# Kernel optimization log

Hardware: AMD Instinct MI355X
Metric: run time of the kernel (lower is better)

The kernel has to match this reference:

```python
import jax, jax.numpy as jnp
import numpy as np

WS, SHIFT, HEADS, FEAT = 7, 3, 3, 56
N = WS * WS

def _rel_pos_index(ws):
    coords = np.stack(np.meshgrid(np.arange(ws), np.arange(ws), indexing='ij'))  # 2,ws,ws
    coords = coords.reshape(2, -1)
    rel = coords[:, :, None] - coords[:, None, :]            # 2,N,N
    rel = rel.transpose(1, 2, 0).astype(np.int64)            # N,N,2
    rel[:, :, 0] += ws - 1
    rel[:, :, 1] += ws - 1
    rel[:, :, 0] *= 2 * ws - 1
    return rel.sum(-1)                                       # N,N in [0,(2ws-1)^2)

def _shift_mask(H, ws, shift):
    img = np.zeros((H, H), dtype=np.float32)
    cnt = 0
    for hs in (slice(0, -ws), slice(-ws, -shift), slice(-shift, None)):
        for wl in (slice(0, -ws), slice(-ws, -shift), slice(-shift, None)):
            img[hs, wl] = cnt
            cnt += 1
    win = img.reshape(H // ws, ws, H // ws, ws).transpose(0, 2, 1, 3).reshape(-1, ws * ws)
    diff = win[:, None, :] - win[:, :, None]                 # nW,N,N (unsqueeze(1)-unsqueeze(2))
    return np.where(diff != 0, -100.0, 0.0).astype(np.float32)

_REL_IDX = jnp.asarray(_rel_pos_index(WS))
_MASK = jnp.asarray(_shift_mask(FEAT, WS, SHIFT))            # (nW_per_img, N, N)

def setup_inputs() -> dict:
    key = jax.random.key(0)
    ks = jax.random.split(key, 4)
    C = 96
    return {
        'x': jax.random.normal(ks[0], (128, C, FEAT, FEAT), jnp.float32),
        'ln_g': jnp.ones((C,), jnp.float32),
        'ln_b': jnp.zeros((C,), jnp.float32),
        'qkv_w': jax.random.normal(ks[1], (3 * C, C), jnp.float32) * 0.02,
        'qkv_b': jnp.zeros((3 * C,), jnp.float32),
        'proj_w': jax.random.normal(ks[2], (C, C), jnp.float32) * 0.02,
        'proj_b': jnp.zeros((C,), jnp.float32),
        'rel_table': jax.random.normal(ks[3], ((2 * WS - 1) ** 2, HEADS), jnp.float32) * 0.02,
    }

def reference(x, ln_g, ln_b, qkv_w, qkv_b, proj_w, proj_b, rel_table):
    B, C, H, W = x.shape
    hd = C // HEADS
    nwh = H // WS
    # BCHW -> BHWC, LayerNorm over C
    xt = x.transpose(0, 2, 3, 1)
    mu = xt.mean(-1, keepdims=True)
    var = ((xt - mu) ** 2).mean(-1, keepdims=True)
    xn = (xt - mu) * jax.lax.rsqrt(var + 1e-5) * ln_g + ln_b
    # cyclic shift
    xn = jnp.roll(xn, (-SHIFT, -SHIFT), axis=(1, 2))
    # window partition -> (B*nW, N, C)
    win = xn.reshape(B, nwh, WS, nwh, WS, C).transpose(0, 1, 3, 2, 4, 5).reshape(-1, N, C)
    # qkv
    qkv = (win @ qkv_w.T + qkv_b).reshape(-1, N, 3, HEADS, hd).transpose(2, 0, 3, 1, 4)
    q, k, v = qkv[0], qkv[1], qkv[2]                         # (B*nW, heads, N, hd)
    attn = jnp.einsum('whid,whjd->whij', q * (hd ** -0.5), k)
    bias = rel_table[_REL_IDX].transpose(2, 0, 1)            # heads,N,N
    attn = attn + bias[None]
    nWp = nwh * nwh
    attn = attn.reshape(B, nWp, HEADS, N, N) + _MASK[None, :, None]
    attn = jax.nn.softmax(attn, axis=-1).reshape(-1, HEADS, N, N)
    out = jnp.einsum('whij,whjd->whid', attn, v).transpose(0, 2, 1, 3).reshape(-1, N, C)
    out = out @ proj_w.T + proj_b
    # window reverse + unshift
    out = out.reshape(B, nwh, nwh, WS, WS, C).transpose(0, 1, 3, 2, 4, 5).reshape(B, H, W, C)
    out = jnp.roll(out, (SHIFT, SHIFT), axis=(1, 2))
    return out.transpose(0, 3, 1, 2)
```

## Files before the change

kernel.cpp:

```cpp
#include <hip/hip_runtime.h>

typedef unsigned short u16;
typedef __bf16 bf8v __attribute__((ext_vector_type(8)));
typedef float f4v __attribute__((ext_vector_type(4)));
typedef f4v __attribute__((may_alias)) f4va;

#define NTOK   49
#define NPAD   64
#define CDIM   96
#define FEAT_  56
#define HWIM   3136
#define SHIFT_ 3

#define WIN_ELEMS (128 * 64 * 49 * 96)
#define QW_ELEMS  (288 * 96)
#define PW_ELEMS  (96 * 96)
#define WS_NEEDED ((size_t)(WIN_ELEMS + QW_ELEMS + PW_ELEMS) * 2)

__device__ __forceinline__ float b2f(u16 u) {
  unsigned v = ((unsigned)u) << 16;
  return __builtin_bit_cast(float, v);
}
__device__ __forceinline__ u16 f2b(float f) {
  return __builtin_bit_cast(u16, (__bf16)f);
}
__device__ __forceinline__ bf8v fragld(const u16* p) {
  return __builtin_bit_cast(bf8v, *(const f4va*)p);
}
__device__ __forceinline__ bf8v cvt8(const float* p) {
  f4v a = *(const f4va*)p;
  f4v b = *(const f4va*)(p + 4);
  union { u16 u[8]; bf8v v; } r;
#pragma unroll
  for (int j = 0; j < 4; ++j) { r.u[j] = f2b(a[j]); r.u[4 + j] = f2b(b[j]); }
  return r.v;
}
__device__ __forceinline__ f4v mfma16(bf8v a, bf8v b, f4v c) {
  return __builtin_amdgcn_mfma_f32_16x16x32_bf16(a, b, c, 0, 0, 0);
}
__device__ __forceinline__ int reg3(int g) { return g < 49 ? 0 : (g < 53 ? 1 : 2); }

__global__ __launch_bounds__(256)
void swin_wcvt(const float* __restrict__ qw, const float* __restrict__ pw,
               u16* __restrict__ qwb, u16* __restrict__ pwb) {
  int i = blockIdx.x * 256 + threadIdx.x;
  if (i < QW_ELEMS) qwb[i] = f2b(qw[i]);
  else              pwb[i - QW_ELEMS] = f2b(pw[i - QW_ELEMS]);
}

__global__ __launch_bounds__(256, 4)
void swin_ln_pack(const float* __restrict__ x,
                  const float* __restrict__ lng, const float* __restrict__ lnb,
                  u16* __restrict__ winbuf) {
  __shared__ __align__(16) float xf[CDIM][60];
  __shared__ __align__(16) u16 wtile[FEAT_][104];
  __shared__ float ps[4][64], pq[4][64];
  __shared__ float gw[CDIM], bw[CDIM];

  const int bid = blockIdx.x;
  const int b = bid / FEAT_, hs = bid - b * FEAT_;
  int h = hs + SHIFT_; if (h >= FEAT_) h -= FEAT_;
  const int tid = threadIdx.x, wv = tid >> 6, lane = tid & 63;

  for (int i = tid; i < CDIM; i += 256) { gw[i] = lng[i]; bw[i] = lnb[i]; }

  const float* base = x + (size_t)b * CDIM * HWIM + h * FEAT_;
  if (lane < 56) {
    const int g = lane / 14, p4 = lane - g * 14;
    for (int i = 0; i < 6; ++i) {
      int c = wv * 24 + i * 4 + g;
      *(f4va*)&xf[c][p4 * 4] = *(const f4va*)(base + (size_t)c * HWIM + p4 * 4);
    }
  }
  __syncthreads();

  const int ws = lane;
  int wsrc = ws + SHIFT_; if (wsrc >= FEAT_) wsrc -= FEAT_;
  float s = 0.f, q = 0.f;
  if (ws < FEAT_)
    for (int i = 0; i < 24; ++i) {
      float v = xf[wv * 24 + i][wsrc];
      s += v; q += v * v;
    }
  ps[wv][lane] = s; pq[wv][lane] = q;
  __syncthreads();

  if (ws < FEAT_) {
    float ts = ps[0][ws] + ps[1][ws] + ps[2][ws] + ps[3][ws];
    float tq = pq[0][ws] + pq[1][ws] + pq[2][ws] + pq[3][ws];
    float m = ts * (1.f / 96.f);
    float r = rsqrtf(tq * (1.f / 96.f) - m * m + 1e-5f);
    for (int i = 0; i < 24; ++i) {
      int c = wv * 24 + i;
      wtile[ws][c] = f2b((xf[c][wsrc] - m) * r * gw[c] + bw[c]);
    }
  }
  __syncthreads();

  const int wrow = hs / 7, tr = hs - wrow * 7;
  for (int idx = tid; idx < 672; idx += 256) {
    int ww = idx / 84, r = idx - ww * 84;
    int wl = r / 12, cc = r - wl * 12;
    u16* dst = winbuf + ((size_t)((b * 64 + wrow * 8 + ww) * 49 + tr * 7)) * CDIM + r * 8;
    *(f4va*)dst = *(const f4va*)&wtile[ww * 7 + wl][cc * 8];
  }
}

__global__ __launch_bounds__(256, 3)
void swin_attn(u16* __restrict__ winbuf,
               const u16* __restrict__ qwb, const u16* __restrict__ pwb,
               const float* __restrict__ qbv, const float* __restrict__ pbv,
               const float* __restrict__ rel) {
  __shared__ __align__(16) u16 qk[NPAD][200];
  __shared__ __align__(16) u16 vt[3][32][72];
  __shared__ __align__(16) u16 Pl[NPAD][72];
  __shared__ float rel_f[507];
  __shared__ float pb_f[CDIM];
  __shared__ float qb_f[3 * CDIM];

  const int blk = blockIdx.x;
  const int wi = blk & 63;
  const int whb = wi >> 3, wwb = wi & 7;
  const int tid = threadIdx.x;
  const int wv = tid >> 6, lane = tid & 63;
  const int quad = lane >> 4, l15 = lane & 15;

  u16* wbase = winbuf + (size_t)blk * (NTOK * CDIM);

  for (int idx = tid; idx < 588; idx += 256) {
    int row = idx / 12, cc = idx - row * 12;
    *(f4va*)&qk[row][cc * 8] = *(const f4va*)(wbase + idx * 8);
  }
  {
    f4v z = {0.f, 0.f, 0.f, 0.f};
    for (int idx = tid; idx < 180; idx += 256) {
      int row = 49 + idx / 12, cc = idx - (idx / 12) * 12;
      *(f4va*)&qk[row][cc * 8] = z;
    }
  }
  for (int i = tid; i < 507; i += 256) rel_f[i] = rel[i];
  for (int i = tid; i < 3 * CDIM; i += 256) qb_f[i] = qbv[i];
  for (int i = tid; i < CDIM; i += 256) pb_f[i] = pbv[i];
  __syncthreads();

  {
    bf8v a[4][3];
    for (int mt = 0; mt < 4; ++mt)
      for (int kt = 0; kt < 3; ++kt)
        a[mt][kt] = fragld(&qk[mt * 16 + l15][kt * 32 + quad * 8]);
    __syncthreads();
    const float qscale = 0.17677669529663687f;
    for (int nt = wv; nt < 18; nt += 4) {
      int n = nt * 16 + l15;
      bf8v bf[3];
      for (int kt = 0; kt < 3; ++kt)
        bf[kt] = fragld(qwb + n * CDIM + kt * 32 + quad * 8);
      float bias = qb_f[n];
      for (int mt = 0; mt < 4; ++mt) {
        f4v c = {0.f, 0.f, 0.f, 0.f};
        c = mfma16(a[mt][0], bf[0], c);
        c = mfma16(a[mt][1], bf[1], c);
        c = mfma16(a[mt][2], bf[2], c);
        for (int rg = 0; rg < 4; ++rg) {
          int m = mt * 16 + quad * 4 + rg;
          float v = c[rg] + bias;
          if (n < 96)        qk[m][n] = f2b(v * qscale);
          else if (n < 192)  qk[m][n] = f2b(v);
          else               vt[(n - 192) >> 5][(n - 192) & 31][m] = f2b(v);
        }
      }
    }
  }
  __syncthreads();

  {
    const int rbase = wv * 16 + quad * 4;
    int rcnt[4], ri_[4], ci_[4];
    for (int rg = 0; rg < 4; ++rg) {
      int r = rbase + rg; if (r > 48) r = 48;
      int ri = r / 7, ci = r - ri * 7;
      ri_[rg] = ri; ci_[rg] = ci;
      rcnt[rg] = reg3(whb * 7 + ri) * 3 + reg3(wwb * 7 + ci);
    }
    int ib_[4][4]; float ms_[4][4]; bool jv_[4];
    for (int nt = 0; nt < 4; ++nt) {
      int j = nt * 16 + l15;
      jv_[nt] = (j < NTOK);
      int rj = j / 7, cj = j - rj * 7;
      int jcnt = reg3(whb * 7 + rj) * 3 + reg3(wwb * 7 + cj);
      for (int rg = 0; rg < 4; ++rg) {
        ib_[nt][rg] = ((ri_[rg] - rj + 6) * 13 + (ci_[rg] - cj + 6)) * 3;
        ms_[nt][rg] = (jcnt != rcnt[rg]) ? -100.f : 0.f;
      }
    }
    for (int h = 0; h < 3; ++h) {
      bf8v aq = fragld(&qk[wv * 16 + l15][h * 32 + quad * 8]);
      f4v S[4];
      for (int nt = 0; nt < 4; ++nt) {
        bf8v bk = fragld(&qk[nt * 16 + l15][96 + h * 32 + quad * 8]);
        f4v z = {0.f, 0.f, 0.f, 0.f};
        S[nt] = mfma16(aq, bk, z);
      }
      for (int nt = 0; nt < 4; ++nt) {
        if (jv_[nt]) {
          for (int rg = 0; rg < 4; ++rg)
            S[nt][rg] += rel_f[ib_[nt][rg] + h] + ms_[nt][rg];
        } else {
          for (int rg = 0; rg < 4; ++rg) S[nt][rg] = -1e30f;
        }
      }
      float inv[4];
      for (int rg = 0; rg < 4; ++rg) {
        float m = fmaxf(fmaxf(S[0][rg], S[1][rg]), fmaxf(S[2][rg], S[3][rg]));
        for (int off = 1; off < 16; off <<= 1) m = fmaxf(m, __shfl_xor(m, off, 64));
        float s = 0.f;
        for (int nt = 0; nt < 4; ++nt) {
          float e = __expf(S[nt][rg] - m); S[nt][rg] = e; s += e;
        }
        for (int off = 1; off < 16; off <<= 1) s += __shfl_xor(s, off, 64);
        inv[rg] = 1.f / s;
      }
      for (int nt = 0; nt < 4; ++nt) {
        int j = nt * 16 + l15;
        for (int rg = 0; rg < 4; ++rg)
          Pl[rbase + rg][j] = f2b(S[nt][rg] * inv[rg]);
      }
      bf8v ap0 = fragld(&Pl[wv * 16 + l15][quad * 8]);
      bf8v ap1 = fragld(&Pl[wv * 16 + l15][32 + quad * 8]);
      for (int nt = 0; nt < 2; ++nt) {
        bf8v bv0 = fragld(&vt[h][nt * 16 + l15][quad * 8]);
        bf8v bv1 = fragld(&vt[h][nt * 16 + l15][32 + quad * 8]);
        f4v c = {0.f, 0.f, 0.f, 0.f};
        c = mfma16(ap0, bv0, c);
        c = mfma16(ap1, bv1, c);
        for (int rg = 0; rg < 4; ++rg)
          qk[rbase + rg][h * 32 + nt * 16 + l15] = f2b(c[rg]);
      }
    }
  }
  __syncthreads();

  {
    bf8v a[4][3];
    for (int mt = 0; mt < 4; ++mt)
      for (int kt = 0; kt < 3; ++kt)
        a[mt][kt] = fragld(&qk[mt * 16 + l15][kt * 32 + quad * 8]);
    __syncthreads();
    for (int nt = wv; nt < 6; nt += 4) {
      int n = nt * 16 + l15;
      bf8v bf[3];
      for (int kt = 0; kt < 3; ++kt)
        bf[kt] = fragld(pwb + n * CDIM + kt * 32 + quad * 8);
      float bias = pb_f[n];
      for (int mt = 0; mt < 4; ++mt) {
        f4v c = {0.f, 0.f, 0.f, 0.f};
        c = mfma16(a[mt][0], bf[0], c);
        c = mfma16(a[mt][1], bf[1], c);
        c = mfma16(a[mt][2], bf[2], c);
        for (int rg = 0; rg < 4; ++rg)
          qk[mt * 16 + quad * 4 + rg][n] = f2b(c[rg] + bias);
      }
    }
  }
  __syncthreads();

  for (int idx = tid; idx < 588; idx += 256) {
    int row = idx / 12, cc = idx - row * 12;
    *(f4va*)(wbase + idx * 8) = *(const f4va*)&qk[row][cc * 8];
  }
}

__global__ __launch_bounds__(256, 4)
void swin_unpack(const u16* __restrict__ winbuf, float* __restrict__ out) {
  __shared__ __align__(16) u16 wtile[FEAT_][104];
  const int bid = blockIdx.x;
  const int b = bid / FEAT_, h = bid - b * FEAT_;
  int hs = h - SHIFT_; if (hs < 0) hs += FEAT_;
  const int wrow = hs / 7, tr = hs - wrow * 7;
  const int tid = threadIdx.x, wv = tid >> 6, lane = tid & 63;

  for (int idx = tid; idx < 672; idx += 256) {
    int ww = idx / 84, r = idx - ww * 84;
    const u16* src = winbuf + ((size_t)((b * 64 + wrow * 8 + ww) * 49 + tr * 7)) * CDIM + r * 8;
    int wl = r / 12, cc = r - wl * 12;
    int ws = ww * 7 + wl;
    int w = ws + SHIFT_; if (w >= FEAT_) w -= FEAT_;
    *(f4va*)&wtile[w][cc * 8] = *(const f4va*)src;
  }
  __syncthreads();
  if (lane < 56) {
    const int g = lane / 14, p4 = lane - g * 14;
    float* obase = out + (size_t)b * CDIM * HWIM + h * FEAT_ + p4 * 4;
    for (int i = 0; i < 6; ++i) {
      int c = wv * 24 + i * 4 + g;
      f4v v;
#pragma unroll
      for (int j = 0; j < 4; ++j) v[j] = b2f(wtile[p4 * 4 + j][c]);
      *(f4va*)(obase + (size_t)c * HWIM) = v;
    }
  }
}

__global__ __launch_bounds__(256, 2)
void swin_fused_fb(const float* __restrict__ x,
                   const float* __restrict__ lng, const float* __restrict__ lnb,
                   const float* __restrict__ qw,  const float* __restrict__ qbv,
                   const float* __restrict__ pw,  const float* __restrict__ pbv,
                   const float* __restrict__ rel,
                   float* __restrict__ out) {
  __shared__ union { float xf[NTOK][97]; u16 qk[NPAD][200]; } A;
  __shared__ union { u16 win16[NPAD][104]; u16 outb[NPAD][98]; } Bu;
  __shared__ u16 vt[3][32][72];
  __shared__ u16 Pl[NPAD][72];
  __shared__ u16 att[NPAD][104];
  __shared__ float gw[CDIM], bwt[CDIM];
  __shared__ float rel_f[507];
  __shared__ float pb_f[CDIM];
  __shared__ float qb_f[3 * CDIM];

  const int blk = blockIdx.x;
  const int b = blk >> 6, wi = blk & 63;
  const int whb = wi >> 3, wwb = wi & 7;
  const int tid = threadIdx.x, wv = tid >> 6, lane = tid & 63;
  const int quad = lane >> 4, l15 = lane & 15;
  {
    int p = lane;
    if (p < NTOK) {
      int r = p / 7, cw = p - r * 7;
      int h = whb * 7 + r + SHIFT_;  if (h >= FEAT_) h -= FEAT_;
      int w = wwb * 7 + cw + SHIFT_; if (w >= FEAT_) w -= FEAT_;
      const float* xp = x + b * CDIM * HWIM + h * FEAT_ + w;
      for (int c = wv; c < CDIM; c += 4) A.xf[p][c] = xp[c * HWIM];
    }
    for (int i = tid; i < CDIM; i += 256) { gw[i] = lng[i]; bwt[i] = lnb[i]; pb_f[i] = pbv[i]; }
    for (int i = tid; i < 507; i += 256) rel_f[i] = rel[i];
    for (int i = tid; i < 3 * CDIM; i += 256) qb_f[i] = qbv[i];
  }
  __syncthreads();
  {
    int p = wv * 16 + (lane >> 2), cg = lane & 3;
    float s = 0.f, q = 0.f;
    if (p < NTOK)
      for (int i = 0; i < 24; ++i) { float v = A.xf[p][cg * 24 + i]; s += v; q += v * v; }
    s += __shfl_xor(s, 1, 64); s += __shfl_xor(s, 2, 64);
    q += __shfl_xor(q, 1, 64); q += __shfl_xor(q, 2, 64);
    float m = s * (1.f / 96.f);
    float r = rsqrtf(q * (1.f / 96.f) - m * m + 1e-5f);
    for (int i = 0; i < 24; ++i) {
      int c = cg * 24 + i;
      float v = (p < NTOK) ? (A.xf[p][c] - m) * r * gw[c] + bwt[c] : 0.f;
      Bu.win16[p][c] = f2b(v);
    }
  }
  __syncthreads();
  {
    bf8v a[4][3];
    for (int mt = 0; mt < 4; ++mt)
      for (int kt = 0; kt < 3; ++kt)
        a[mt][kt] = fragld(&Bu.win16[mt * 16 + l15][kt * 32 + quad * 8]);
    const float qscale = 0.17677669529663687f;
    for (int nt = wv; nt < 18; nt += 4) {
      int n = nt * 16 + l15;
      const float* wr = qw + n * CDIM;
      bf8v bf[3];
      for (int kt = 0; kt < 3; ++kt) bf[kt] = cvt8(wr + kt * 32 + quad * 8);
      float bias = qb_f[n];
      for (int mt = 0; mt < 4; ++mt) {
        f4v c = {0.f, 0.f, 0.f, 0.f};
        c = mfma16(a[mt][0], bf[0], c);
        c = mfma16(a[mt][1], bf[1], c);
        c = mfma16(a[mt][2], bf[2], c);
        for (int rg = 0; rg < 4; ++rg) {
          int m = mt * 16 + quad * 4 + rg;
          float v = c[rg] + bias;
          if (n < 96)        A.qk[m][n] = f2b(v * qscale);
          else if (n < 192)  A.qk[m][n] = f2b(v);
          else               vt[(n - 192) >> 5][(n - 192) & 31][m] = f2b(v);
        }
      }
    }
  }
  __syncthreads();
  {
    const int rbase = wv * 16 + quad * 4;
    int rcnt[4], ri_[4], ci_[4];
    for (int rg = 0; rg < 4; ++rg) {
      int r = rbase + rg; if (r > 48) r = 48;
      int ri = r / 7, ci = r - ri * 7;
      ri_[rg] = ri; ci_[rg] = ci;
      rcnt[rg] = reg3(whb * 7 + ri) * 3 + reg3(wwb * 7 + ci);
    }
    for (int h = 0; h < 3; ++h) {
      bf8v aq = fragld(&A.qk[wv * 16 + l15][h * 32 + quad * 8]);
      f4v S[4];
      for (int nt = 0; nt < 4; ++nt) {
        bf8v bk = fragld(&A.qk[nt * 16 + l15][96 + h * 32 + quad * 8]);
        f4v z = {0.f, 0.f, 0.f, 0.f};
        S[nt] = mfma16(aq, bk, z);
      }
      for (int nt = 0; nt < 4; ++nt) {
        int j = nt * 16 + l15;
        if (j < NTOK) {
          int rj = j / 7, cj = j - rj * 7;
          int jcnt = reg3(whb * 7 + rj) * 3 + reg3(wwb * 7 + cj);
          for (int rg = 0; rg < 4; ++rg) {
            float add = rel_f[((ri_[rg] - rj + 6) * 13 + (ci_[rg] - cj + 6)) * 3 + h];
            if (jcnt != rcnt[rg]) add -= 100.f;
            S[nt][rg] += add;
          }
        } else {
          for (int rg = 0; rg < 4; ++rg) S[nt][rg] = -1e30f;
        }
      }
      float inv[4];
      for (int rg = 0; rg < 4; ++rg) {
        float m = fmaxf(fmaxf(S[0][rg], S[1][rg]), fmaxf(S[2][rg], S[3][rg]));
        for (int off = 1; off < 16; off <<= 1) m = fmaxf(m, __shfl_xor(m, off, 64));
        float s = 0.f;
        for (int nt = 0; nt < 4; ++nt) { float e = __expf(S[nt][rg] - m); S[nt][rg] = e; s += e; }
        for (int off = 1; off < 16; off <<= 1) s += __shfl_xor(s, off, 64);
        inv[rg] = 1.f / s;
      }
      for (int nt = 0; nt < 4; ++nt) {
        int j = nt * 16 + l15;
        for (int rg = 0; rg < 4; ++rg) Pl[rbase + rg][j] = f2b(S[nt][rg] * inv[rg]);
      }
      bf8v ap0 = fragld(&Pl[wv * 16 + l15][quad * 8]);
      bf8v ap1 = fragld(&Pl[wv * 16 + l15][32 + quad * 8]);
      for (int nt = 0; nt < 2; ++nt) {
        bf8v bv0 = fragld(&vt[h][nt * 16 + l15][quad * 8]);
        bf8v bv1 = fragld(&vt[h][nt * 16 + l15][32 + quad * 8]);
        f4v c = {0.f, 0.f, 0.f, 0.f};
        c = mfma16(ap0, bv0, c);
        c = mfma16(ap1, bv1, c);
        for (int rg = 0; rg < 4; ++rg)
          att[rbase + rg][h * 32 + nt * 16 + l15] = f2b(c[rg]);
      }
    }
  }
  __syncthreads();
  {
    bf8v a[4][3];
    for (int mt = 0; mt < 4; ++mt)
      for (int kt = 0; kt < 3; ++kt)
        a[mt][kt] = fragld(&att[mt * 16 + l15][kt * 32 + quad * 8]);
    for (int nt = wv; nt < 6; nt += 4) {
      int n = nt * 16 + l15;
      const float* wr = pw + n * CDIM;
      bf8v bf[3];
      for (int kt = 0; kt < 3; ++kt) bf[kt] = cvt8(wr + kt * 32 + quad * 8);
      float bias = pb_f[n];
      for (int mt = 0; mt < 4; ++mt) {
        f4v c = {0.f, 0.f, 0.f, 0.f};
        c = mfma16(a[mt][0], bf[0], c);
        c = mfma16(a[mt][1], bf[1], c);
        c = mfma16(a[mt][2], bf[2], c);
        for (int rg = 0; rg < 4; ++rg)
          Bu.outb[mt * 16 + quad * 4 + rg][n] = f2b(c[rg] + bias);
      }
    }
  }
  __syncthreads();
  {
    int p = lane;
    if (p < NTOK) {
      int r = p / 7, cw = p - r * 7;
      int h = whb * 7 + r + SHIFT_;  if (h >= FEAT_) h -= FEAT_;
      int w = wwb * 7 + cw + SHIFT_; if (w >= FEAT_) w -= FEAT_;
      float* op = out + b * CDIM * HWIM + h * FEAT_ + w;
      for (int c = wv; c < CDIM; c += 4) op[c * HWIM] = b2f(Bu.outb[p][c]);
    }
  }
}

extern "C" void kernel_launch(void* const* d_in, const int* in_sizes, int n_in,
                              void* d_out, int out_size, void* d_ws, size_t ws_size,
                              hipStream_t stream) {
  (void)in_sizes; (void)n_in; (void)out_size;
  const float* x   = (const float*)d_in[0];
  const float* lng = (const float*)d_in[1];
  const float* lnb = (const float*)d_in[2];
  const float* qw  = (const float*)d_in[3];
  const float* qbv = (const float*)d_in[4];
  const float* pw  = (const float*)d_in[5];
  const float* pbv = (const float*)d_in[6];
  const float* rel = (const float*)d_in[7];
  float* out = (float*)d_out;

  if (ws_size >= WS_NEEDED) {
    u16* winbuf = (u16*)d_ws;
    u16* qwb = winbuf + WIN_ELEMS;
    u16* pwb = qwb + QW_ELEMS;
    swin_wcvt<<<dim3(144), dim3(256), 0, stream>>>(qw, pw, qwb, pwb);
    swin_ln_pack<<<dim3(128 * FEAT_), dim3(256), 0, stream>>>(x, lng, lnb, winbuf);
    swin_attn<<<dim3(8192), dim3(256), 0, stream>>>(winbuf, qwb, pwb, qbv, pbv, rel);
    swin_unpack<<<dim3(128 * FEAT_), dim3(256), 0, stream>>>(winbuf, out);
  } else {
    swin_fused_fb<<<dim3(8192), dim3(256), 0, stream>>>(x, lng, lnb, qw, qbv, pw, pbv, rel, out);
  }
}
```

Baseline: 495.4 us.

## Vectorize LDS stores via swapped MFMA operands, direct LN writes, permuted unpack tile

The LayerNorm pack kernel now writes normalized bf16 rows straight to global memory in 16-byte chunks, dropping the shared staging tile and one barrier, and spreads its input load over all threads. The attention kernel swaps MFMA operand order so each lane holds four consecutive columns, which allows packed 8-byte shared-memory stores for Q/K, P, attention output and projection output. The same change lets the softmax reduction use two cross-lane shuffles instead of four per row. The projection work is split evenly across the four waves, and the unpack kernel permutes its tile rows to cut LDS bank conflicts; occupancy hints are raised on the pack and unpack kernels.

```diff
diff --git a/kernel.cpp b/kernel.cpp
--- a/kernel.cpp
+++ b/kernel.cpp
@@ -4,6 +4,8 @@
 typedef __bf16 bf8v __attribute__((ext_vector_type(8)));
 typedef float f4v __attribute__((ext_vector_type(4)));
 typedef f4v __attribute__((may_alias)) f4va;
+typedef unsigned int u2v __attribute__((ext_vector_type(2)));
+typedef u2v __attribute__((may_alias)) u2va;
 
 #define NTOK   49
 #define NPAD   64
@@ -48,12 +50,11 @@
   else              pwb[i - QW_ELEMS] = f2b(pw[i - QW_ELEMS]);
 }
 
-__global__ __launch_bounds__(256, 4)
+__global__ __launch_bounds__(256, 6)
 void swin_ln_pack(const float* __restrict__ x,
                   const float* __restrict__ lng, const float* __restrict__ lnb,
                   u16* __restrict__ winbuf) {
   __shared__ __align__(16) float xf[CDIM][60];
-  __shared__ __align__(16) u16 wtile[FEAT_][104];
   __shared__ float ps[4][64], pq[4][64];
   __shared__ float gw[CDIM], bw[CDIM];
 
@@ -65,12 +66,9 @@
   for (int i = tid; i < CDIM; i += 256) { gw[i] = lng[i]; bw[i] = lnb[i]; }
 
   const float* base = x + (size_t)b * CDIM * HWIM + h * FEAT_;
-  if (lane < 56) {
-    const int g = lane / 14, p4 = lane - g * 14;
-    for (int i = 0; i < 6; ++i) {
-      int c = wv * 24 + i * 4 + g;
-      *(f4va*)&xf[c][p4 * 4] = *(const f4va*)(base + (size_t)c * HWIM + p4 * 4);
-    }
+  for (int idx = tid; idx < 1344; idx += 256) {
+    int c = idx / 14, p4 = idx - c * 14;
+    *(f4va*)&xf[c][p4 * 4] = *(const f4va*)(base + (size_t)c * HWIM + p4 * 4);
   }
   __syncthreads();
 
@@ -90,19 +88,17 @@
     float tq = pq[0][ws] + pq[1][ws] + pq[2][ws] + pq[3][ws];
     float m = ts * (1.f / 96.f);
     float r = rsqrtf(tq * (1.f / 96.f) - m * m + 1e-5f);
+    const int ww = ws / 7, wl = ws - ww * 7;
+    const int wrow = hs / 7, tr = hs - wrow * 7;
+    u16* dst = winbuf + ((size_t)((b * 64 + wrow * 8 + ww) * 49 + tr * 7 + wl)) * CDIM + wv * 24;
+    union { u16 u[24]; f4v d[3]; } pk;
+#pragma unroll
     for (int i = 0; i < 24; ++i) {
       int c = wv * 24 + i;
-      wtile[ws][c] = f2b((xf[c][wsrc] - m) * r * gw[c] + bw[c]);
-    }
-  }
-  __syncthreads();
-
-  const int wrow = hs / 7, tr = hs - wrow * 7;
-  for (int idx = tid; idx < 672; idx += 256) {
-    int ww = idx / 84, r = idx - ww * 84;
-    int wl = r / 12, cc = r - wl * 12;
-    u16* dst = winbuf + ((size_t)((b * 64 + wrow * 8 + ww) * 49 + tr * 7)) * CDIM + r * 8;
-    *(f4va*)dst = *(const f4va*)&wtile[ww * 7 + wl][cc * 8];
+      pk.u[i] = f2b((xf[c][wsrc] - m) * r * gw[c] + bw[c]);
+    }
+#pragma unroll
+    for (int j = 0; j < 3; ++j) *(f4va*)(dst + j * 8) = pk.d[j];
   }
 }
 
@@ -115,8 +111,8 @@
   __shared__ __align__(16) u16 vt[3][32][72];
   __shared__ __align__(16) u16 Pl[NPAD][72];
   __shared__ float rel_f[507];
-  __shared__ float pb_f[CDIM];
-  __shared__ float qb_f[3 * CDIM];
+  __shared__ __align__(16) float pb_f[CDIM];
+  __shared__ __align__(16) float qb_f[3 * CDIM];
 
   const int blk = blockIdx.x;
   const int wi = blk & 63;
@@ -155,86 +151,107 @@
       bf8v bf[3];
       for (int kt = 0; kt < 3; ++kt)
         bf[kt] = fragld(qwb + n * CDIM + kt * 32 + quad * 8);
-      float bias = qb_f[n];
-      for (int mt = 0; mt < 4; ++mt) {
-        f4v c = {0.f, 0.f, 0.f, 0.f};
-        c = mfma16(a[mt][0], bf[0], c);
-        c = mfma16(a[mt][1], bf[1], c);
-        c = mfma16(a[mt][2], bf[2], c);
-        for (int rg = 0; rg < 4; ++rg) {
-          int m = mt * 16 + quad * 4 + rg;
-          float v = c[rg] + bias;
-          if (n < 96)        qk[m][n] = f2b(v * qscale);
-          else if (n < 192)  qk[m][n] = f2b(v);
-          else               vt[(n - 192) >> 5][(n - 192) & 31][m] = f2b(v);
+      if (nt < 12) {
+        const int n0 = nt * 16 + quad * 4;
+        f4v bias = *(const f4va*)&qb_f[n0];
+        const bool isq = (nt < 6);
+        for (int mt = 0; mt < 4; ++mt) {
+          f4v c = {0.f, 0.f, 0.f, 0.f};
+          c = mfma16(bf[0], a[mt][0], c);
+          c = mfma16(bf[1], a[mt][1], c);
+          c = mfma16(bf[2], a[mt][2], c);
+          union { u16 u[4]; u2v d; } pk;
+#pragma unroll
+          for (int rg = 0; rg < 4; ++rg) {
+            float v = c[rg] + bias[rg];
+            if (isq) v *= qscale;
+            pk.u[rg] = f2b(v);
+          }
+          *(u2va*)&qk[mt * 16 + l15][n0] = pk.d;
         }
-      }
-    }
-  }
-  __syncthreads();
-
-  {
-    const int rbase = wv * 16 + quad * 4;
-    int rcnt[4], ri_[4], ci_[4];
-    for (int rg = 0; rg < 4; ++rg) {
-      int r = rbase + rg; if (r > 48) r = 48;
-      int ri = r / 7, ci = r - ri * 7;
-      ri_[rg] = ri; ci_[rg] = ci;
-      rcnt[rg] = reg3(whb * 7 + ri) * 3 + reg3(wwb * 7 + ci);
-    }
-    int ib_[4][4]; float ms_[4][4]; bool jv_[4];
-    for (int nt = 0; nt < 4; ++nt) {
-      int j = nt * 16 + l15;
-      jv_[nt] = (j < NTOK);
-      int rj = j / 7, cj = j - rj * 7;
-      int jcnt = reg3(whb * 7 + rj) * 3 + reg3(wwb * 7 + cj);
+      } else {
+        float bias = qb_f[n];
+        const int hd = (n - 192) >> 5, dc = (n - 192) & 31;
+        for (int mt = 0; mt < 4; ++mt) {
+          f4v c = {0.f, 0.f, 0.f, 0.f};
+          c = mfma16(a[mt][0], bf[0], c);
+          c = mfma16(a[mt][1], bf[1], c);
+          c = mfma16(a[mt][2], bf[2], c);
+          union { u16 u[4]; u2v d; } pk;
+#pragma unroll
+          for (int rg = 0; rg < 4; ++rg) pk.u[rg] = f2b(c[rg] + bias);
+          *(u2va*)&vt[hd][dc][mt * 16 + quad * 4] = pk.d;
+        }
+      }
+    }
+  }
+  __syncthreads();
+
+  {
+    const int mrow = wv * 16 + l15;
+    int mc = mrow > 48 ? 48 : mrow;
+    const int ri = mc / 7, ci = mc - ri * 7;
+    const int rcnt = reg3(whb * 7 + ri) * 3 + reg3(wwb * 7 + ci);
+    int ib_[4][4]; float ms_[4][4]; bool jv_[4][4];
+    for (int jt = 0; jt < 4; ++jt)
       for (int rg = 0; rg < 4; ++rg) {
-        ib_[nt][rg] = ((ri_[rg] - rj + 6) * 13 + (ci_[rg] - cj + 6)) * 3;
-        ms_[nt][rg] = (jcnt != rcnt[rg]) ? -100.f : 0.f;
-      }
-    }
+        int j = jt * 16 + quad * 4 + rg;
+        jv_[jt][rg] = (j < NTOK);
+        int jj = j > 48 ? 48 : j;
+        int rj = jj / 7, cj = jj - rj * 7;
+        int jcnt = reg3(whb * 7 + rj) * 3 + reg3(wwb * 7 + cj);
+        ib_[jt][rg] = ((ri - rj + 6) * 13 + (ci - cj + 6)) * 3;
+        ms_[jt][rg] = (jcnt != rcnt) ? -100.f : 0.f;
+      }
     for (int h = 0; h < 3; ++h) {
       bf8v aq = fragld(&qk[wv * 16 + l15][h * 32 + quad * 8]);
       f4v S[4];
-      for (int nt = 0; nt < 4; ++nt) {
-        bf8v bk = fragld(&qk[nt * 16 + l15][96 + h * 32 + quad * 8]);
+      for (int jt = 0; jt < 4; ++jt) {
+        bf8v bk = fragld(&qk[jt * 16 + l15][96 + h * 32 + quad * 8]);
         f4v z = {0.f, 0.f, 0.f, 0.f};
-        S[nt] = mfma16(aq, bk, z);
-      }
-      for (int nt = 0; nt < 4; ++nt) {
-        if (jv_[nt]) {
-          for (int rg = 0; rg < 4; ++rg)
-            S[nt][rg] += rel_f[ib_[nt][rg] + h] + ms_[nt][rg];
-        } else {
-          for (int rg = 0; rg < 4; ++rg) S[nt][rg] = -1e30f;
+        S[jt] = mfma16(bk, aq, z);
+      }
+      for (int jt = 0; jt < 4; ++jt)
+#pragma unroll
+        for (int rg = 0; rg < 4; ++rg) {
+          if (jv_[jt][rg]) S[jt][rg] += rel_f[ib_[jt][rg] + h] + ms_[jt][rg];
+          else             S[jt][rg] = -1e30f;
         }
-      }
-      float inv[4];
-      for (int rg = 0; rg < 4; ++rg) {
-        float m = fmaxf(fmaxf(S[0][rg], S[1][rg]), fmaxf(S[2][rg], S[3][rg]));
-        for (int off = 1; off < 16; off <<= 1) m = fmaxf(m, __shfl_xor(m, off, 64));
-        float s = 0.f;
-        for (int nt = 0; nt < 4; ++nt) {
-          float e = __expf(S[nt][rg] - m); S[nt][rg] = e; s += e;
-        }
-        for (int off = 1; off < 16; off <<= 1) s += __shfl_xor(s, off, 64);
-        inv[rg] = 1.f / s;
-      }
-      for (int nt = 0; nt < 4; ++nt) {
-        int j = nt * 16 + l15;
-        for (int rg = 0; rg < 4; ++rg)
-          Pl[rbase + rg][j] = f2b(S[nt][rg] * inv[rg]);
+      float mx0 = fmaxf(fmaxf(S[0][0], S[0][1]), fmaxf(S[0][2], S[0][3]));
+      float mx1 = fmaxf(fmaxf(S[1][0], S[1][1]), fmaxf(S[1][2], S[1][3]));
+      float mx2 = fmaxf(fmaxf(S[2][0], S[2][1]), fmaxf(S[2][2], S[2][3]));
+      float mx3 = fmaxf(fmaxf(S[3][0], S[3][1]), fmaxf(S[3][2], S[3][3]));
+      float mx = fmaxf(fmaxf(mx0, mx1), fmaxf(mx2, mx3));
+      mx = fmaxf(mx, __shfl_xor(mx, 16, 64));
+      mx = fmaxf(mx, __shfl_xor(mx, 32, 64));
+      float s = 0.f;
+      for (int jt = 0; jt < 4; ++jt) {
+        float e0 = __expf(S[jt][0] - mx), e1 = __expf(S[jt][1] - mx);
+        float e2 = __expf(S[jt][2] - mx), e3 = __expf(S[jt][3] - mx);
+        S[jt][0] = e0; S[jt][1] = e1; S[jt][2] = e2; S[jt][3] = e3;
+        s += (e0 + e1) + (e2 + e3);
+      }
+      s += __shfl_xor(s, 16, 64);
+      s += __shfl_xor(s, 32, 64);
+      float inv = 1.f / s;
+      for (int jt = 0; jt < 4; ++jt) {
+        union { u16 u[4]; u2v d; } pk;
+#pragma unroll
+        for (int rg = 0; rg < 4; ++rg) pk.u[rg] = f2b(S[jt][rg] * inv);
+        *(u2va*)&Pl[mrow][jt * 16 + quad * 4] = pk.d;
       }
       bf8v ap0 = fragld(&Pl[wv * 16 + l15][quad * 8]);
       bf8v ap1 = fragld(&Pl[wv * 16 + l15][32 + quad * 8]);
-      for (int nt = 0; nt < 2; ++nt) {
-        bf8v bv0 = fragld(&vt[h][nt * 16 + l15][quad * 8]);
-        bf8v bv1 = fragld(&vt[h][nt * 16 + l15][32 + quad * 8]);
+      for (int dt = 0; dt < 2; ++dt) {
+        bf8v bv0 = fragld(&vt[h][dt * 16 + l15][quad * 8]);
+        bf8v bv1 = fragld(&vt[h][dt * 16 + l15][32 + quad * 8]);
         f4v c = {0.f, 0.f, 0.f, 0.f};
-        c = mfma16(ap0, bv0, c);
-        c = mfma16(ap1, bv1, c);
-        for (int rg = 0; rg < 4; ++rg)
-          qk[rbase + rg][h * 32 + nt * 16 + l15] = f2b(c[rg]);
+        c = mfma16(bv0, ap0, c);
+        c = mfma16(bv1, ap1, c);
+        union { u16 u[4]; u2v d; } pk;
+#pragma unroll
+        for (int rg = 0; rg < 4; ++rg) pk.u[rg] = f2b(c[rg]);
+        *(u2va*)&qk[mrow][h * 32 + dt * 16 + quad * 4] = pk.d;
       }
     }
   }
@@ -246,20 +263,25 @@
       for (int kt = 0; kt < 3; ++kt)
         a[mt][kt] = fragld(&qk[mt * 16 + l15][kt * 32 + quad * 8]);
     __syncthreads();
-    for (int nt = wv; nt < 6; nt += 4) {
-      int n = nt * 16 + l15;
-      bf8v bf[3];
-      for (int kt = 0; kt < 3; ++kt)
-        bf[kt] = fragld(pwb + n * CDIM + kt * 32 + quad * 8);
-      float bias = pb_f[n];
-      for (int mt = 0; mt < 4; ++mt) {
-        f4v c = {0.f, 0.f, 0.f, 0.f};
-        c = mfma16(a[mt][0], bf[0], c);
-        c = mfma16(a[mt][1], bf[1], c);
-        c = mfma16(a[mt][2], bf[2], c);
-        for (int rg = 0; rg < 4; ++rg)
-          qk[mt * 16 + quad * 4 + rg][n] = f2b(c[rg] + bias);
-      }
+    int lastnt = -1;
+    bf8v bf[3]; f4v bias = {0.f, 0.f, 0.f, 0.f};
+    for (int u = wv * 6; u < wv * 6 + 6; ++u) {
+      int nt = u >> 2, mt = u & 3;
+      if (nt != lastnt) {
+        lastnt = nt;
+        int n = nt * 16 + l15;
+        for (int kt = 0; kt < 3; ++kt)
+          bf[kt] = fragld(pwb + n * CDIM + kt * 32 + quad * 8);
+        bias = *(const f4va*)&pb_f[nt * 16 + quad * 4];
+      }
+      f4v c = {0.f, 0.f, 0.f, 0.f};
+      c = mfma16(bf[0], a[mt][0], c);
+      c = mfma16(bf[1], a[mt][1], c);
+      c = mfma16(bf[2], a[mt][2], c);
+      union { u16 u[4]; u2v d; } pk;
+#pragma unroll
+      for (int rg = 0; rg < 4; ++rg) pk.u[rg] = f2b(c[rg] + bias[rg]);
+      *(u2va*)&qk[mt * 16 + l15][nt * 16 + quad * 4] = pk.d;
     }
   }
   __syncthreads();
@@ -270,9 +292,9 @@
   }
 }
 
-__global__ __launch_bounds__(256, 4)
+__global__ __launch_bounds__(256, 8)
 void swin_unpack(const u16* __restrict__ winbuf, float* __restrict__ out) {
-  __shared__ __align__(16) u16 wtile[FEAT_][104];
+  __shared__ __align__(16) u16 wtile[64][104];
   const int bid = blockIdx.x;
   const int b = bid / FEAT_, h = bid - b * FEAT_;
   int hs = h - SHIFT_; if (hs < 0) hs += FEAT_;
@@ -285,7 +307,8 @@
     int wl = r / 12, cc = r - wl * 12;
     int ws = ww * 7 + wl;
     int w = ws + SHIFT_; if (w >= FEAT_) w -= FEAT_;
-    *(f4va*)&wtile[w][cc * 8] = *(const f4va*)src;
+    int sr = (w >> 2) | ((w & 3) << 4);
+    *(f4va*)&wtile[sr][cc * 8] = *(const f4va*)src;
   }
   __syncthreads();
   if (lane < 56) {
@@ -295,7 +318,7 @@
       int c = wv * 24 + i * 4 + g;
       f4v v;
 #pragma unroll
-      for (int j = 0; j < 4; ++j) v[j] = b2f(wtile[p4 * 4 + j][c]);
+      for (int j = 0; j < 4; ++j) v[j] = b2f(wtile[p4 + 16 * j][c]);
       *(f4va*)(obase + (size_t)c * HWIM) = v;
     }
   }
```

After: 543.5 us. +9.7%, slower.
